# Optimization experiments

Measured on AMD Instinct MI355X. Metric: run time of the kernel, lower is better.

## Reference

```python
import jax, jax.numpy as jnp
import numpy as np

N = 8192
IN_F = 64
OUT_F = 64
D_INT = 32
ALPHA = 0.2  # LeakyReLU negative slope


def setup_inputs() -> dict:
    key = jax.random.key(0)
    k1, k2, k3, k4 = jax.random.split(key, 4)
    x = jax.random.normal(k1, (N, IN_F), dtype=jnp.float32)
    adj = jnp.ones((N, N), dtype=bool)  # unused by the original forward math
    intent_embeds = jax.random.normal(k2, (N, D_INT), dtype=jnp.float32)
    # Xavier-uniform-like init scales (gain 1.414)
    limW = 1.414 * np.sqrt(6.0 / (IN_F + OUT_F))
    W = jax.random.uniform(k3, (IN_F, OUT_F), dtype=jnp.float32, minval=-limW, maxval=limW)
    a_len = 2 * OUT_F + 2 * D_INT
    lima = 1.414 * np.sqrt(6.0 / (a_len + 1))
    a = jax.random.uniform(k4, (a_len, 1), dtype=jnp.float32, minval=-lima, maxval=lima)
    return {"input": x, "adj": adj, "intent_embeds": intent_embeds, "W": W, "a": a}


def reference(input, adj, intent_embeds, W, a):
    # h: [N, F]
    h = input @ W
    F_ = h.shape[1]
    a = a[:, 0]
    a_src, a_dst = a[:F_], a[F_:2 * F_]
    b_src, b_dst = a[2 * F_:2 * F_ + D_INT], a[2 * F_ + D_INT:]
    # Additive score decomposes exactly: e[i,j] = lrelu(s_i + t_j)
    s = h @ a_src + intent_embeds @ b_src          # [N]
    t = h @ a_dst + intent_embeds @ b_dst          # [N]
    e = jax.nn.leaky_relu(s[:, None] + t[None, :], negative_slope=ALPHA)  # [N, N]
    # NOTE: original applies softmax over dim=0 (source axis), no adj masking
    attention = jax.nn.softmax(e, axis=0)
    h_prime = attention @ h                        # [N, F]
    return jax.nn.elu(h_prime)
```

## Files before the change

### kernel.cpp

```cpp
#include <hip/hip_runtime.h>
#include <cstdint>
#include <cstddef>

#define N_NODES 8192
#define F_OUT   64
#define DINT    32
#define ALPHA   0.2f

__global__ __launch_bounds__(64) void k_h_st(
    const float* __restrict__ x, const float* __restrict__ ie,
    const float* __restrict__ W, const float* __restrict__ a,
    float* __restrict__ h, float* __restrict__ s, float* __restrict__ t)
{
    const int i = blockIdx.x;
    const int f = threadIdx.x;
    const float* xr = x + (size_t)i * 64;

    float acc = 0.f;
    #pragma unroll 16
    for (int k = 0; k < 64; ++k)
        acc = fmaf(xr[k], W[k * 64 + f], acc);

    h[(size_t)i * 64 + f] = acc;

    float ps = acc * a[f];
    float pt = acc * a[64 + f];
    if (f < DINT) {
        float e = ie[(size_t)i * DINT + f];
        ps = fmaf(e, a[128 + f], ps);
        pt = fmaf(e, a[160 + f], pt);
    }
    #pragma unroll
    for (int m = 1; m < 64; m <<= 1) {
        ps += __shfl_xor(ps, m, 64);
        pt += __shfl_xor(pt, m, 64);
    }
    if (f == 0) { s[i] = ps; t[i] = pt; }
}

__global__ __launch_bounds__(256) void k_smax(
    const float* __restrict__ s, float* __restrict__ smax)
{
    float m = -1e30f;
    for (int i = threadIdx.x; i < N_NODES; i += 256)
        m = fmaxf(m, s[i]);
    #pragma unroll
    for (int off = 32; off; off >>= 1)
        m = fmaxf(m, __shfl_down(m, off, 64));
    __shared__ float red[4];
    if ((threadIdx.x & 63) == 0) red[threadIdx.x >> 6] = m;
    __syncthreads();
    if (threadIdx.x == 0)
        smax[0] = fmaxf(fmaxf(red[0], red[1]), fmaxf(red[2], red[3]));
}

__global__ __launch_bounds__(256) void k_ranks(
    const float* __restrict__ s, const float* __restrict__ t,
    const float* __restrict__ smax_p,
    int* __restrict__ rank_s, int* __restrict__ pos,
    int* __restrict__ rank_t, int* __restrict__ q,
    float* __restrict__ se1, float* __restrict__ se2)
{
    const int wave = threadIdx.x >> 6, lane = threadIdx.x & 63;
    const int idx = blockIdx.x * 4 + wave;
    const int which = blockIdx.y;
    int c1 = 0, c2 = 0;
    if (which == 0) {
        const float si = s[idx], nsi = -si;
        for (int k = lane; k < N_NODES; k += 64) {
            float sk = s[k];
            c1 += (sk < si) || (sk == si && k < idx);
            c2 += (t[k] < nsi);
        }
    } else {
        const float tj = t[idx], ntj = -tj;
        for (int k = lane; k < N_NODES; k += 64) {
            float tk = t[k];
            c1 += (tk < tj) || (tk == tj && k < idx);
            c2 += (s[k] < ntj);
        }
    }
    int p = c1 * 16384 + c2;
    #pragma unroll
    for (int m = 1; m < 64; m <<= 1) p += __shfl_xor(p, m, 64);
    if (lane == 0) {
        int r1 = p >> 14, r2 = p & 16383;
        if (which == 0) {
            rank_s[idx] = r1;
            pos[idx] = r2;
            float d = s[idx] - smax_p[0];
            se1[r1] = __expf(d);
            se2[r1] = __expf(ALPHA * d);
        } else {
            rank_t[idx] = r1;
            q[idx] = r2;
        }
    }
}

__global__ __launch_bounds__(1024) void k_scanP(
    const float* __restrict__ se1, const float* __restrict__ se2,
    float* __restrict__ SufP1, float* __restrict__ PreP2)
{
    __shared__ double sc[1024];
    const int tid = threadIdx.x;
    double loc[8], sum;

    sum = 0.0;
    #pragma unroll
    for (int k = 0; k < 8; ++k) { loc[k] = (double)se2[tid * 8 + k]; sum += loc[k]; }
    sc[tid] = sum; __syncthreads();
    for (int off = 1; off < 1024; off <<= 1) {
        double v = (tid >= off) ? sc[tid - off] : 0.0;
        __syncthreads();
        sc[tid] += v;
        __syncthreads();
    }
    {
        double run = sc[tid] - sum;
        #pragma unroll
        for (int k = 0; k < 8; ++k) { PreP2[tid * 8 + k] = (float)run; run += loc[k]; }
        if (tid == 1023) PreP2[8192] = (float)run;
    }
    __syncthreads();

    sum = 0.0;
    #pragma unroll
    for (int k = 0; k < 8; ++k) { loc[k] = (double)se1[tid * 8 + k]; sum += loc[k]; }
    sc[tid] = sum; __syncthreads();
    for (int off = 1; off < 1024; off <<= 1) {
        double v = (tid >= off) ? sc[tid - off] : 0.0;
        __syncthreads();
        sc[tid] += v;
        __syncthreads();
    }
    {
        double acc = sc[1023] - sc[tid];
        #pragma unroll
        for (int k = 7; k >= 0; --k) { acc += loc[k]; SufP1[tid * 8 + k] = (float)acc; }
        if (tid == 1023) SufP1[8192] = 0.f;
    }
}

__global__ __launch_bounds__(256) void k_coef(
    const float* __restrict__ h, const float* __restrict__ t,
    const float* __restrict__ smax_p,
    const int* __restrict__ rank_t, const int* __restrict__ q,
    const float* __restrict__ SufP1, const float* __restrict__ PreP2,
    float* __restrict__ G1, float* __restrict__ G2)
{
    const int j = blockIdx.x * 4 + (threadIdx.x >> 6);
    const int f = threadIdx.x & 63;
    const float smax = smax_p[0];
    const float zc = smax + t[j];
    const float c = fmaxf(zc, ALPHA * zc);
    const float pe = zc - c;
    const float ne = ALPHA * zc - c;
    const int qj = q[j];
    const float E1 = __expf(pe), E2 = __expf(ne);
    const float D = E1 * SufP1[qj] + E2 * PreP2[qj];
    const float invD = 1.f / D;
    const float hv = h[(size_t)j * 64 + f];
    const int r = rank_t[j];
    G1[(size_t)r * 64 + f] = (E1 * invD) * hv;
    G2[(size_t)r * 64 + f] = (E2 * invD) * hv;
}

__global__ __launch_bounds__(256) void k_tilesum(
    const float* __restrict__ G1, const float* __restrict__ G2,
    float* __restrict__ T1, float* __restrict__ T2)
{
    const int tile = blockIdx.x;
    const int arr  = blockIdx.y;
    const float* G = arr ? G2 : G1;
    float* T = arr ? T2 : T1;
    const int f = threadIdx.x & 63, seg = threadIdx.x >> 6;
    const int r0 = tile * 128 + seg * 32;
    float acc = 0.f;
    for (int r = 0; r < 32; ++r) acc += G[(size_t)(r0 + r) * 64 + f];
    __shared__ float red[4][64];
    red[seg][f] = acc; __syncthreads();
    if (seg == 0) T[tile * 64 + f] = red[0][f] + red[1][f] + red[2][f] + red[3][f];
}

__global__ __launch_bounds__(128) void k_tilescan(
    const float* __restrict__ T1, const float* __restrict__ T2,
    float* __restrict__ O1, float* __restrict__ O2)
{
    const int tid = threadIdx.x;
    if (tid < 64) {
        float acc = 0.f;
        for (int t = 63; t >= 0; --t) { O1[t * 64 + tid] = acc; acc += T1[t * 64 + tid]; }
    } else {
        const int f = tid - 64;
        float acc = 0.f;
        for (int t = 0; t < 64; ++t) { O2[t * 64 + f] = acc; acc += T2[t * 64 + f]; }
    }
}

__global__ __launch_bounds__(64) void k_scan2(
    float* __restrict__ G1, float* __restrict__ G2,
    const float* __restrict__ O1, const float* __restrict__ O2)
{
    const int tile = blockIdx.x, arr = blockIdx.y, f = threadIdx.x;
    if (arr == 0) {
        float acc = O1[tile * 64 + f];
        if (tile == 63) G1[(size_t)8192 * 64 + f] = 0.f;
        for (int rb = 15; rb >= 0; --rb) {
            const int r0 = tile * 128 + rb * 8;
            float v[8];
            #pragma unroll
            for (int k = 0; k < 8; ++k) v[k] = G1[(size_t)(r0 + k) * 64 + f];
            #pragma unroll
            for (int k = 7; k >= 0; --k) { acc += v[k]; G1[(size_t)(r0 + k) * 64 + f] = acc; }
        }
    } else {
        float acc = O2[tile * 64 + f];
        for (int rb = 0; rb < 16; ++rb) {
            const int r0 = tile * 128 + rb * 8;
            float v[8];
            #pragma unroll
            for (int k = 0; k < 8; ++k) v[k] = G2[(size_t)(r0 + k) * 64 + f];
            #pragma unroll
            for (int k = 0; k < 8; ++k) { float old = v[k]; G2[(size_t)(r0 + k) * 64 + f] = acc; acc += old; }
        }
        if (tile == 63) G2[(size_t)8192 * 64 + f] = acc;
    }
}

__global__ __launch_bounds__(256) void k_out(
    const float* __restrict__ s, const float* __restrict__ smax_p,
    const int* __restrict__ pos,
    const float* __restrict__ G1, const float* __restrict__ G2,
    float* __restrict__ out)
{
    const int i = blockIdx.x * 4 + (threadIdx.x >> 6);
    const int f = threadIdx.x & 63;
    const float d = s[i] - smax_p[0];
    const float e1 = __expf(d), e2 = __expf(ALPHA * d);
    const int p = pos[i];
    float v = e1 * G1[(size_t)p * 64 + f] + e2 * G2[(size_t)p * 64 + f];
    out[(size_t)i * 64 + f] = v > 0.f ? v : expm1f(v);
}

extern "C" void kernel_launch(void* const* d_in, const int* in_sizes, int n_in,
                              void* d_out, int out_size, void* d_ws, size_t ws_size,
                              hipStream_t stream)
{
    const float* x  = (const float*)d_in[0];
    const float* ie = (const float*)d_in[2];
    const float* W  = (const float*)d_in[3];
    const float* a  = (const float*)d_in[4];
    float* out = (float*)d_out;

    float* p = (float*)d_ws;
    float* h     = p; p += (size_t)N_NODES * F_OUT;
    float* s     = p; p += N_NODES;
    float* t     = p; p += N_NODES;
    float* smax  = p; p += 16;
    float* se1   = p; p += N_NODES;
    float* se2   = p; p += N_NODES;
    float* SufP1 = p; p += N_NODES + 16;
    float* PreP2 = p; p += N_NODES + 16;
    float* T1    = p; p += 64 * 64;
    float* T2    = p; p += 64 * 64;
    float* O1    = p; p += 64 * 64;
    float* O2    = p; p += 64 * 64;
    float* G1    = p; p += (size_t)(N_NODES + 1) * F_OUT + 48;
    float* G2    = p; p += (size_t)(N_NODES + 1) * F_OUT + 48;
    int* rank_s  = (int*)p; p += N_NODES;
    int* rank_t  = (int*)p; p += N_NODES;
    int* pos     = (int*)p; p += N_NODES;
    int* q       = (int*)p; p += N_NODES;

    k_h_st    <<<N_NODES, 64, 0, stream>>>(x, ie, W, a, h, s, t);
    k_smax    <<<1, 256, 0, stream>>>(s, smax);
    k_ranks   <<<dim3(N_NODES / 4, 2), 256, 0, stream>>>(s, t, smax,
                      rank_s, pos, rank_t, q, se1, se2);
    k_scanP   <<<1, 1024, 0, stream>>>(se1, se2, SufP1, PreP2);
    k_coef    <<<N_NODES / 4, 256, 0, stream>>>(h, t, smax, rank_t, q,
                      SufP1, PreP2, G1, G2);
    k_tilesum <<<dim3(64, 2), 256, 0, stream>>>(G1, G2, T1, T2);
    k_tilescan<<<1, 128, 0, stream>>>(T1, T2, O1, O2);
    k_scan2   <<<dim3(64, 2), 64, 0, stream>>>(G1, G2, O1, O2);
    k_out     <<<N_NODES / 4, 256, 0, stream>>>(s, smax, pos, G1, G2, out);
}
```

Measured before the change: 379.7 us.

## Fuse smax into rank kernel, merge scan/coef stages, drop G materialization

```diff
diff --git a/kernel.cpp b/kernel.cpp
--- a/kernel.cpp
+++ b/kernel.cpp
@@ -38,69 +38,92 @@
     if (f == 0) { s[i] = ps; t[i] = pt; }
 }
 
-__global__ __launch_bounds__(256) void k_smax(
-    const float* __restrict__ s, float* __restrict__ smax)
-{
-    float m = -1e30f;
-    for (int i = threadIdx.x; i < N_NODES; i += 256)
-        m = fmaxf(m, s[i]);
-    #pragma unroll
-    for (int off = 32; off; off >>= 1)
-        m = fmaxf(m, __shfl_down(m, off, 64));
-    __shared__ float red[4];
-    if ((threadIdx.x & 63) == 0) red[threadIdx.x >> 6] = m;
-    __syncthreads();
-    if (threadIdx.x == 0)
-        smax[0] = fmaxf(fmaxf(red[0], red[1]), fmaxf(red[2], red[3]));
-}
-
 __global__ __launch_bounds__(256) void k_ranks(
     const float* __restrict__ s, const float* __restrict__ t,
-    const float* __restrict__ smax_p,
-    int* __restrict__ rank_s, int* __restrict__ pos,
-    int* __restrict__ rank_t, int* __restrict__ q,
+    float* __restrict__ smax,
+    int* __restrict__ pos, int* __restrict__ inv_t,
+    float* __restrict__ t_sorted, int* __restrict__ q_sorted,
     float* __restrict__ se1, float* __restrict__ se2)
 {
+    __shared__ __align__(16) float s_sh[2048];
+    __shared__ __align__(16) float t_sh[2048];
     const int wave = threadIdx.x >> 6, lane = threadIdx.x & 63;
     const int idx = blockIdx.x * 4 + wave;
     const int which = blockIdx.y;
+
+    const float key = (which == 0) ? s[idx] : t[idx];
+    const float nkey = -key;
     int c1 = 0, c2 = 0;
+    float m = -1e30f;
+
+    for (int c = 0; c < 4; ++c) {
+        const int base = c * 2048;
+        #pragma unroll
+        for (int l = 0; l < 2; ++l) {
+            int o = threadIdx.x * 4 + l * 1024;
+            *reinterpret_cast<float4*>(&s_sh[o]) =
+                *reinterpret_cast<const float4*>(&s[base + o]);
+            *reinterpret_cast<float4*>(&t_sh[o]) =
+                *reinterpret_cast<const float4*>(&t[base + o]);
+        }
+        __syncthreads();
+
+        if (which == 0) {
+            for (int k = lane * 4; k < 2048; k += 256) {
+                float4 sv = *reinterpret_cast<const float4*>(&s_sh[k]);
+                float4 tv = *reinterpret_cast<const float4*>(&t_sh[k]);
+                const int k0 = base + k;
+                c1 += (sv.x < key) || (sv.x == key && (k0 + 0) < idx);
+                c1 += (sv.y < key) || (sv.y == key && (k0 + 1) < idx);
+                c1 += (sv.z < key) || (sv.z == key && (k0 + 2) < idx);
+                c1 += (sv.w < key) || (sv.w == key && (k0 + 3) < idx);
+                c2 += (tv.x < nkey) + (tv.y < nkey) + (tv.z < nkey) + (tv.w < nkey);
+                m = fmaxf(m, fmaxf(fmaxf(sv.x, sv.y), fmaxf(sv.z, sv.w)));
+            }
+        } else {
+            for (int k = lane * 4; k < 2048; k += 256) {
+                float4 tv = *reinterpret_cast<const float4*>(&t_sh[k]);
+                float4 sv = *reinterpret_cast<const float4*>(&s_sh[k]);
+                const int k0 = base + k;
+                c1 += (tv.x < key) || (tv.x == key && (k0 + 0) < idx);
+                c1 += (tv.y < key) || (tv.y == key && (k0 + 1) < idx);
+                c1 += (tv.z < key) || (tv.z == key && (k0 + 2) < idx);
+                c1 += (tv.w < key) || (tv.w == key && (k0 + 3) < idx);
+                c2 += (sv.x < nkey) + (sv.y < nkey) + (sv.z < nkey) + (sv.w < nkey);
+            }
+        }
+        __syncthreads();
+    }
+
+    int p = c1 * 16384 + c2;
+    #pragma unroll
+    for (int mm = 1; mm < 64; mm <<= 1) p += __shfl_xor(p, mm, 64);
+
     if (which == 0) {
-        const float si = s[idx], nsi = -si;
-        for (int k = lane; k < N_NODES; k += 64) {
-            float sk = s[k];
-            c1 += (sk < si) || (sk == si && k < idx);
-            c2 += (t[k] < nsi);
-        }
-    } else {
-        const float tj = t[idx], ntj = -tj;
-        for (int k = lane; k < N_NODES; k += 64) {
-            float tk = t[k];
-            c1 += (tk < tj) || (tk == tj && k < idx);
-            c2 += (s[k] < ntj);
-        }
-    }
-    int p = c1 * 16384 + c2;
-    #pragma unroll
-    for (int m = 1; m < 64; m <<= 1) p += __shfl_xor(p, m, 64);
-    if (lane == 0) {
-        int r1 = p >> 14, r2 = p & 16383;
-        if (which == 0) {
-            rank_s[idx] = r1;
+        #pragma unroll
+        for (int mm = 1; mm < 64; mm <<= 1) m = fmaxf(m, __shfl_xor(m, mm, 64));
+        if (lane == 0) {
+            const int r1 = p >> 14, r2 = p & 16383;
             pos[idx] = r2;
-            float d = s[idx] - smax_p[0];
+            const float d = key - m;
             se1[r1] = __expf(d);
             se2[r1] = __expf(ALPHA * d);
-        } else {
-            rank_t[idx] = r1;
-            q[idx] = r2;
-        }
-    }
-}
-
-__global__ __launch_bounds__(1024) void k_scanP(
+            if (idx == 0) smax[0] = m;
+        }
+    } else if (lane == 0) {
+        const int r1 = p >> 14, r2 = p & 16383;
+        inv_t[r1] = idx;
+        t_sorted[r1] = key;
+        q_sorted[r1] = r2;
+    }
+}
+
+__global__ __launch_bounds__(1024) void k_mid(
     const float* __restrict__ se1, const float* __restrict__ se2,
-    float* __restrict__ SufP1, float* __restrict__ PreP2)
+    const float* __restrict__ smax_p,
+    const float* __restrict__ t_sorted, const int* __restrict__ q_sorted,
+    float* __restrict__ SufP1, float* __restrict__ PreP2,
+    float* __restrict__ cf1, float* __restrict__ cf2)
 {
     __shared__ double sc[1024];
     const int tid = threadIdx.x;
@@ -140,98 +163,92 @@
         for (int k = 7; k >= 0; --k) { acc += loc[k]; SufP1[tid * 8 + k] = (float)acc; }
         if (tid == 1023) SufP1[8192] = 0.f;
     }
-}
-
-__global__ __launch_bounds__(256) void k_coef(
-    const float* __restrict__ h, const float* __restrict__ t,
-    const float* __restrict__ smax_p,
-    const int* __restrict__ rank_t, const int* __restrict__ q,
-    const float* __restrict__ SufP1, const float* __restrict__ PreP2,
-    float* __restrict__ G1, float* __restrict__ G2)
-{
-    const int j = blockIdx.x * 4 + (threadIdx.x >> 6);
-    const int f = threadIdx.x & 63;
+
+    __threadfence();
+    __syncthreads();
+
     const float smax = smax_p[0];
-    const float zc = smax + t[j];
-    const float c = fmaxf(zc, ALPHA * zc);
-    const float pe = zc - c;
-    const float ne = ALPHA * zc - c;
-    const int qj = q[j];
-    const float E1 = __expf(pe), E2 = __expf(ne);
-    const float D = E1 * SufP1[qj] + E2 * PreP2[qj];
-    const float invD = 1.f / D;
-    const float hv = h[(size_t)j * 64 + f];
-    const int r = rank_t[j];
-    G1[(size_t)r * 64 + f] = (E1 * invD) * hv;
-    G2[(size_t)r * 64 + f] = (E2 * invD) * hv;
+    #pragma unroll
+    for (int k = 0; k < 8; ++k) {
+        const int r = tid + k * 1024;
+        const float tj = t_sorted[r];
+        const float zc = smax + tj;
+        const float c = fmaxf(zc, ALPHA * zc);
+        const float E1 = __expf(zc - c);
+        const float E2 = __expf(ALPHA * zc - c);
+        const int qj = q_sorted[r];
+        const float D = E1 * SufP1[qj] + E2 * PreP2[qj];
+        const float invD = 1.f / D;
+        cf1[r] = E1 * invD;
+        cf2[r] = E2 * invD;
+    }
 }
 
 __global__ __launch_bounds__(256) void k_tilesum(
-    const float* __restrict__ G1, const float* __restrict__ G2,
+    const float* __restrict__ h, const int* __restrict__ inv_t,
+    const float* __restrict__ cf1, const float* __restrict__ cf2,
     float* __restrict__ T1, float* __restrict__ T2)
 {
     const int tile = blockIdx.x;
-    const int arr  = blockIdx.y;
-    const float* G = arr ? G2 : G1;
-    float* T = arr ? T2 : T1;
-    const int f = threadIdx.x & 63, seg = threadIdx.x >> 6;
-    const int r0 = tile * 128 + seg * 32;
-    float acc = 0.f;
-    for (int r = 0; r < 32; ++r) acc += G[(size_t)(r0 + r) * 64 + f];
-    __shared__ float red[4][64];
-    red[seg][f] = acc; __syncthreads();
-    if (seg == 0) T[tile * 64 + f] = red[0][f] + red[1][f] + red[2][f] + red[3][f];
-}
-
-__global__ __launch_bounds__(128) void k_tilescan(
+    const int wave = threadIdx.x >> 6, f = threadIdx.x & 63;
+    const int r0 = tile * 128 + wave * 32;
+    float a1 = 0.f, a2 = 0.f;
+    for (int k = 0; k < 32; ++k) {
+        const int r = r0 + k;
+        const int j = inv_t[r];
+        const float v = h[(size_t)j * 64 + f];
+        a1 = fmaf(cf1[r], v, a1);
+        a2 = fmaf(cf2[r], v, a2);
+    }
+    __shared__ float red[2][4][64];
+    red[0][wave][f] = a1; red[1][wave][f] = a2;
+    __syncthreads();
+    if (wave == 0)
+        T1[tile * 64 + f] = red[0][0][f] + red[0][1][f] + red[0][2][f] + red[0][3][f];
+    else if (wave == 1)
+        T2[tile * 64 + f] = red[1][0][f] + red[1][1][f] + red[1][2][f] + red[1][3][f];
+}
+
+__global__ __launch_bounds__(64) void k_scan2(
+    const float* __restrict__ h, const int* __restrict__ inv_t,
+    const float* __restrict__ cf1, const float* __restrict__ cf2,
     const float* __restrict__ T1, const float* __restrict__ T2,
-    float* __restrict__ O1, float* __restrict__ O2)
-{
-    const int tid = threadIdx.x;
-    if (tid < 64) {
-        float acc = 0.f;
-        for (int t = 63; t >= 0; --t) { O1[t * 64 + tid] = acc; acc += T1[t * 64 + tid]; }
-    } else {
-        const int f = tid - 64;
-        float acc = 0.f;
-        for (int t = 0; t < 64; ++t) { O2[t * 64 + f] = acc; acc += T2[t * 64 + f]; }
-    }
-}
-
-__global__ __launch_bounds__(64) void k_scan2(
-    float* __restrict__ G1, float* __restrict__ G2,
-    const float* __restrict__ O1, const float* __restrict__ O2)
+    float* __restrict__ S1, float* __restrict__ S2)
 {
     const int tile = blockIdx.x, arr = blockIdx.y, f = threadIdx.x;
     if (arr == 0) {
-        float acc = O1[tile * 64 + f];
-        if (tile == 63) G1[(size_t)8192 * 64 + f] = 0.f;
+        float acc = 0.f;
+        for (int tt = tile + 1; tt < 64; ++tt) acc += T1[tt * 64 + f];
+        if (tile == 63) S1[(size_t)8192 * 64 + f] = 0.f;
         for (int rb = 15; rb >= 0; --rb) {
             const int r0 = tile * 128 + rb * 8;
             float v[8];
             #pragma unroll
-            for (int k = 0; k < 8; ++k) v[k] = G1[(size_t)(r0 + k) * 64 + f];
+            for (int k = 0; k < 8; ++k)
+                v[k] = cf1[r0 + k] * h[(size_t)inv_t[r0 + k] * 64 + f];
             #pragma unroll
-            for (int k = 7; k >= 0; --k) { acc += v[k]; G1[(size_t)(r0 + k) * 64 + f] = acc; }
+            for (int k = 7; k >= 0; --k) { acc += v[k]; S1[(size_t)(r0 + k) * 64 + f] = acc; }
         }
     } else {
-        float acc = O2[tile * 64 + f];
+        float acc = 0.f;
+        for (int tt = 0; tt < tile; ++tt) acc += T2[tt * 64 + f];
         for (int rb = 0; rb < 16; ++rb) {
             const int r0 = tile * 128 + rb * 8;
             float v[8];
             #pragma unroll
-            for (int k = 0; k < 8; ++k) v[k] = G2[(size_t)(r0 + k) * 64 + f];
+            for (int k = 0; k < 8; ++k)
+                v[k] = cf2[r0 + k] * h[(size_t)inv_t[r0 + k] * 64 + f];
             #pragma unroll
-            for (int k = 0; k < 8; ++k) { float old = v[k]; G2[(size_t)(r0 + k) * 64 + f] = acc; acc += old; }
-        }
-        if (tile == 63) G2[(size_t)8192 * 64 + f] = acc;
+            for (int k = 0; k < 8; ++k) { S2[(size_t)(r0 + k) * 64 + f] = acc; acc += v[k]; }
+        }
+        if (tile == 63) S2[(size_t)8192 * 64 + f] = acc;
     }
 }
 
 __global__ __launch_bounds__(256) void k_out(
     const float* __restrict__ s, const float* __restrict__ smax_p,
     const int* __restrict__ pos,
-    const float* __restrict__ G1, const float* __restrict__ G2,
+    const float* __restrict__ S1, const float* __restrict__ S2,
     float* __restrict__ out)
 {
     const int i = blockIdx.x * 4 + (threadIdx.x >> 6);
@@ -239,7 +256,7 @@
     const float d = s[i] - smax_p[0];
     const float e1 = __expf(d), e2 = __expf(ALPHA * d);
     const int p = pos[i];
-    float v = e1 * G1[(size_t)p * 64 + f] + e2 * G2[(size_t)p * 64 + f];
+    const float v = fmaf(e1, S1[(size_t)p * 64 + f], e2 * S2[(size_t)p * 64 + f]);
     out[(size_t)i * 64 + f] = v > 0.f ? v : expm1f(v);
 }
 
@@ -254,34 +271,31 @@
     float* out = (float*)d_out;
 
     float* p = (float*)d_ws;
-    float* h     = p; p += (size_t)N_NODES * F_OUT;
-    float* s     = p; p += N_NODES;
-    float* t     = p; p += N_NODES;
-    float* smax  = p; p += 16;
-    float* se1   = p; p += N_NODES;
-    float* se2   = p; p += N_NODES;
-    float* SufP1 = p; p += N_NODES + 16;
-    float* PreP2 = p; p += N_NODES + 16;
-    float* T1    = p; p += 64 * 64;
-    float* T2    = p; p += 64 * 64;
-    float* O1    = p; p += 64 * 64;
-    float* O2    = p; p += 64 * 64;
-    float* G1    = p; p += (size_t)(N_NODES + 1) * F_OUT + 48;
-    float* G2    = p; p += (size_t)(N_NODES + 1) * F_OUT + 48;
-    int* rank_s  = (int*)p; p += N_NODES;
-    int* rank_t  = (int*)p; p += N_NODES;
-    int* pos     = (int*)p; p += N_NODES;
-    int* q       = (int*)p; p += N_NODES;
+    float* h        = p; p += (size_t)N_NODES * F_OUT;
+    float* s        = p; p += N_NODES;
+    float* t        = p; p += N_NODES;
+    float* smax     = p; p += 16;
+    float* se1      = p; p += N_NODES;
+    float* se2      = p; p += N_NODES;
+    float* SufP1    = p; p += N_NODES + 64;
+    float* PreP2    = p; p += N_NODES + 64;
+    float* t_sorted = p; p += N_NODES;
+    float* cf1      = p; p += N_NODES;
+    float* cf2      = p; p += N_NODES;
+    float* T1       = p; p += 64 * 64;
+    float* T2       = p; p += 64 * 64;
+    float* S1       = p; p += (size_t)(N_NODES + 1) * F_OUT + 64;
+    float* S2       = p; p += (size_t)(N_NODES + 1) * F_OUT + 64;
+    int* pos        = (int*)p; p += N_NODES;
+    int* inv_t      = (int*)p; p += N_NODES;
+    int* q_sorted   = (int*)p; p += N_NODES;
 
     k_h_st    <<<N_NODES, 64, 0, stream>>>(x, ie, W, a, h, s, t);
-    k_smax    <<<1, 256, 0, stream>>>(s, smax);
     k_ranks   <<<dim3(N_NODES / 4, 2), 256, 0, stream>>>(s, t, smax,
-                      rank_s, pos, rank_t, q, se1, se2);
-    k_scanP   <<<1, 1024, 0, stream>>>(se1, se2, SufP1, PreP2);
-    k_coef    <<<N_NODES / 4, 256, 0, stream>>>(h, t, smax, rank_t, q,
-                      SufP1, PreP2, G1, G2);
-    k_tilesum <<<dim3(64, 2), 256, 0, stream>>>(G1, G2, T1, T2);
-    k_tilescan<<<1, 128, 0, stream>>>(T1, T2, O1, O2);
-    k_scan2   <<<dim3(64, 2), 64, 0, stream>>>(G1, G2, O1, O2);
-    k_out     <<<N_NODES / 4, 256, 0, stream>>>(s, smax, pos, G1, G2, out);
-}
+                      pos, inv_t, t_sorted, q_sorted, se1, se2);
+    k_mid     <<<1, 1024, 0, stream>>>(se1, se2, smax, t_sorted, q_sorted,
+                      SufP1, PreP2, cf1, cf2);
+    k_tilesum <<<64, 256, 0, stream>>>(h, inv_t, cf1, cf2, T1, T2);
+    k_scan2   <<<dim3(64, 2), 64, 0, stream>>>(h, inv_t, cf1, cf2, T1, T2, S1, S2);
+    k_out     <<<N_NODES / 4, 256, 0, stream>>>(s, smax, pos, S1, S2, out);
+}
```

New measurement: 385.8 us. About the same (+1.6%).
